# Kernel optimization log

Hardware: AMD Instinct MI355X
Metric: run time of the kernel (lower is better)

The kernel has to match this reference:

```python
import jax, jax.numpy as jnp
import numpy as np

N_MIN = 5
N_MAX = 16
VARIANTS_PER_N = 16
NUM_HIDDEN = 2
HIDDEN = 512
TOTAL_MODELS = (N_MAX - N_MIN + 1) * VARIANTS_PER_N  # 192
BATCH = 65536


def setup_inputs() -> dict:
    key = jax.random.key(0)
    ks = jax.random.split(key, 8)
    n = 16
    s_in = 1.0 / np.sqrt(n)
    s_h = 1.0 / np.sqrt(HIDDEN)
    return {
        "T": jax.random.normal(ks[0], (BATCH, n), dtype=jnp.float32),
        "n": n,
        "variant_index": 3,
        "w_in": jax.random.normal(ks[1], (TOTAL_MODELS, HIDDEN, N_MAX), dtype=jnp.float32) * s_in,
        "b_in": jax.random.normal(ks[2], (TOTAL_MODELS, HIDDEN), dtype=jnp.float32) * 0.01,
        "w_hid": jax.random.normal(ks[3], (TOTAL_MODELS, NUM_HIDDEN, HIDDEN, HIDDEN), dtype=jnp.float32) * s_h,
        "b_hid": jax.random.normal(ks[4], (TOTAL_MODELS, NUM_HIDDEN, HIDDEN), dtype=jnp.float32) * 0.01,
        "w_out": jax.random.normal(ks[5], (TOTAL_MODELS, N_MAX + 1, HIDDEN), dtype=jnp.float32) * s_h,
        "b_out": jax.random.normal(ks[6], (TOTAL_MODELS, N_MAX + 1), dtype=jnp.float32) * 0.01,
    }


def _distortion(X, n):
    # X: (B, n+1). Z[:, n-1-i] = sum_j X[:, j] * X[:, j+i+1] (zero-padded shift).
    # lag k = i+1 -> column n-k; loop is over fixed small n (<=16), unrolls statically.
    cols = [jnp.sum(X[:, :-k] * X[:, k:], axis=1) for k in range(1, n + 1)]
    return jnp.stack(cols[::-1], axis=1)  # (B, n)


def reference(T, n, variant_index, w_in, b_in, w_hid, b_hid, w_out, b_out):
    model_idx = (n - N_MIN) * VARIANTS_PER_N + variant_index
    wi = w_in[model_idx]    # (H, N_MAX)
    bi = b_in[model_idx]    # (H,)
    wh = w_hid[model_idx]   # (2, H, H)
    bh = b_hid[model_idx]   # (2, H)
    wo = w_out[model_idx]   # (N_MAX+1, H)
    bo = b_out[model_idx]   # (N_MAX+1,)

    T_pad = jnp.pad(T, ((0, 0), (0, N_MAX - n)))  # (B, N_MAX)
    norm = jnp.sqrt(jnp.clip(jnp.sum(T_pad * T_pad, axis=1, keepdims=True), 1e-12))
    T_unit = T_pad / norm
    scale = jnp.sqrt(norm)

    x = jax.nn.silu(T_unit @ wi.T + bi)
    for h in range(NUM_HIDDEN):
        x = jax.nn.relu(x @ wh[h].T + bh[h])
    x_full = (x @ wo.T + bo) * scale  # (B, N_MAX+1)

    X_hat = x_full[:, :n + 1]
    X_hat_clamped = jnp.clip(X_hat, -2.0, 2.0)
    error = jnp.mean((_distortion(X_hat, n) - T) ** 2)
    error_clamped = jnp.mean((_distortion(X_hat_clamped, n) - T) ** 2)
    return (X_hat, error, X_hat_clamped, error_clamped)
```

## Files before the change

### kernel.cpp

```cpp
#include <hip/hip_runtime.h>

#define BATCH 65536
#define MT 128
#define NBLK (BATCH / MT)

typedef unsigned short u16;
typedef __bf16 bf16x8 __attribute__((ext_vector_type(8)));
typedef float f32x4 __attribute__((ext_vector_type(4)));

#define WI_OFF 0
#define WH_OFF 16384
#define WO_OFF 540672
#define WS_USH 557056
#define BI_F 0
#define BH_F 512
#define BO_F 1536
#define PART_F 1568
#define PREP_WH 65536
#define PREP_WI 2048
#define PREP_WO 2048
#define PREP_SC 1568
#define PREP_TOTAL (PREP_WH + PREP_WI + PREP_WO + PREP_SC)

__device__ inline u16 f2bf(float f) {
  union { float f; unsigned u; } v; v.f = f;
  unsigned u = v.u + 0x7fffu + ((v.u >> 16) & 1u);
  return (u16)(u >> 16);
}

__global__ void prep_kernel(const float* __restrict__ w_in, const float* __restrict__ b_in,
                            const float* __restrict__ w_hid, const float* __restrict__ b_hid,
                            const float* __restrict__ w_out, const float* __restrict__ b_out,
                            const int* __restrict__ variant, int n,
                            u16* __restrict__ wsu, float* __restrict__ wsf)
{
  const int model = (n - 5) * 16 + variant[0];
  const int i = blockIdx.x * 256 + threadIdx.x;
  if (i < PREP_WH) {
    int g = i & 3, col = (i >> 2) & 511, K32 = (i >> 11) & 15, l = i >> 15;
    const float* src = w_hid + (size_t)model * 524288 + (size_t)l * 262144 + col * 512 + K32 * 32 + g * 8;
    u16* dst = wsu + WH_OFF + (size_t)i * 8;
    #pragma unroll
    for (int e = 0; e < 8; ++e) dst[e] = f2bf(src[e]);
  } else if (i < PREP_WH + PREP_WI) {
    int j = i - PREP_WH;
    int g = j & 3, col = j >> 2;
    u16* dst = wsu + WI_OFF + (size_t)j * 8;
    #pragma unroll
    for (int e = 0; e < 8; ++e) {
      int k = g * 8 + e;
      dst[e] = (k < 16) ? f2bf(w_in[(size_t)model * 8192 + col * 16 + k]) : (u16)0;
    }
  } else if (i < PREP_WH + PREP_WI + PREP_WO) {
    int j = i - PREP_WH - PREP_WI;
    int g = j & 3, col = (j >> 2) & 31, K32 = j >> 7;
    u16* dst = wsu + WO_OFF + (size_t)j * 8;
    #pragma unroll
    for (int e = 0; e < 8; ++e) {
      int k = K32 * 32 + g * 8 + e;
      dst[e] = (col < 17) ? f2bf(w_out[(size_t)model * 8704 + col * 512 + k]) : (u16)0;
    }
  } else if (i < PREP_TOTAL) {
    int j = i - PREP_WH - PREP_WI - PREP_WO;
    if (j < 512)       wsf[BI_F + j] = b_in[(size_t)model * 512 + j];
    else if (j < 1536) wsf[BH_F + (j - 512)] = b_hid[(size_t)model * 1024 + (j - 512)];
    else               { int o = j - 1536; wsf[BO_F + o] = (o < 17) ? b_out[(size_t)model * 17 + o] : 0.f; }
  }
}

__device__ __forceinline__ bf16x8 rdA(const char* xb, int row, int kbyte) {
  return *reinterpret_cast<const bf16x8*>(xb + row * 1024 + (kbyte ^ ((row & 15) << 4)));
}
__device__ __forceinline__ void st16(char* xb, int row, int col, u16 v) {
  *(u16*)(xb + row * 1024 + ((col * 2) ^ ((row & 15) << 4))) = v;
}

template<int NK>
__device__ __forceinline__ void dense_layer(const u16* __restrict__ Wp,
                                            const float* __restrict__ bias, int act,
                                            char* xb, int l15, int q, int r0, int c0)
{
  f32x4 acc[4][8];
  #pragma unroll
  for (int a = 0; a < 4; ++a)
    #pragma unroll
    for (int b = 0; b < 8; ++b) { f32x4 z = {0.f, 0.f, 0.f, 0.f}; acc[a][b] = z; }

  const u16* Wl = Wp + (c0 + l15) * 32 + q * 8;

  if constexpr (NK == 1) {
    uint4 b0[8];
    #pragma unroll
    for (int ct = 0; ct < 8; ++ct)
      b0[ct] = *reinterpret_cast<const uint4*>(Wl + ct * 512);
    const int kb = q * 16;
    #pragma unroll
    for (int mt = 0; mt < 4; ++mt) {
      bf16x8 a = rdA(xb, r0 + mt * 16 + l15, kb);
      #pragma unroll
      for (int ct = 0; ct < 8; ++ct)
        acc[mt][ct] = __builtin_amdgcn_mfma_f32_16x16x32_bf16(
            a, __builtin_bit_cast(bf16x8, b0[ct]), acc[mt][ct], 0, 0, 0);
    }
  } else {
    uint4 bc[8], bn[8];
    #pragma unroll
    for (int ct = 0; ct < 8; ++ct)
      bc[ct] = *reinterpret_cast<const uint4*>(Wl + ct * 512);
    #pragma unroll 1
    for (int i = 0; i < NK; i += 2) {
      {
        const u16* p = Wl + (size_t)(i + 1) * 16384;
        #pragma unroll
        for (int ct = 0; ct < 8; ++ct)
          bn[ct] = *reinterpret_cast<const uint4*>(p + ct * 512);
      }
      {
        const int kb = i * 64 + q * 16;
        #pragma unroll
        for (int mt = 0; mt < 4; ++mt) {
          bf16x8 a = rdA(xb, r0 + mt * 16 + l15, kb);
          #pragma unroll
          for (int ct = 0; ct < 8; ++ct)
            acc[mt][ct] = __builtin_amdgcn_mfma_f32_16x16x32_bf16(
                a, __builtin_bit_cast(bf16x8, bc[ct]), acc[mt][ct], 0, 0, 0);
        }
      }
      {
        const u16* p = Wl + (size_t)((i + 2) & (NK - 1)) * 16384;
        #pragma unroll
        for (int ct = 0; ct < 8; ++ct)
          bc[ct] = *reinterpret_cast<const uint4*>(p + ct * 512);
      }
      {
        const int kb = (i + 1) * 64 + q * 16;
        #pragma unroll
        for (int mt = 0; mt < 4; ++mt) {
          bf16x8 a = rdA(xb, r0 + mt * 16 + l15, kb);
          #pragma unroll
          for (int ct = 0; ct < 8; ++ct)
            acc[mt][ct] = __builtin_amdgcn_mfma_f32_16x16x32_bf16(
                a, __builtin_bit_cast(bf16x8, bn[ct]), acc[mt][ct], 0, 0, 0);
        }
      }
    }
  }
  __syncthreads();

  float bv[8];
  #pragma unroll
  for (int ct = 0; ct < 8; ++ct) bv[ct] = bias[c0 + ct * 16 + l15];
  #pragma unroll
  for (int mt = 0; mt < 4; ++mt)
    #pragma unroll
    for (int ct = 0; ct < 8; ++ct)
      #pragma unroll
      for (int j = 0; j < 4; ++j) {
        int row = r0 + mt * 16 + q * 4 + j;
        float z = acc[mt][ct][j] + bv[ct];
        float h = act ? fmaxf(z, 0.f) : z / (1.f + __expf(-z));
        st16(xb, row, c0 + ct * 16 + l15, f2bf(h));
      }
  __syncthreads();
}

template<int CN>
__global__ __launch_bounds__(512, 2) void fused_kernel(
    const float* __restrict__ T, const u16* __restrict__ wsu,
    const float* __restrict__ wsf, float* __restrict__ Xout, float* __restrict__ Xcout,
    float* __restrict__ errPart, int n_arg)
{
  const int n = CN ? CN : n_arg;
  __shared__ u16 xs[MT * 512];
  __shared__ float xo[MT * 20];
  __shared__ float ts[MT * 16];
  __shared__ float scaleS[MT];
  __shared__ float ered[8][2];

  const int tid = threadIdx.x;
  const int blk = blockIdx.x;
  const int lane = tid & 63;
  const int wid = tid >> 6;
  const int l15 = lane & 15;
  const int q = lane >> 4;
  const int r0 = (wid >> 2) * 64;
  const int c0 = (wid & 3) * 128;
  char* xb = (char*)xs;

  {
    const int r = tid >> 2, j = tid & 3;
    const size_t gr = (size_t)blk * MT + r;
    const float* tp = T + gr * n;
    float v[4]; float ss = 0.f;
    #pragma unroll
    for (int c = 0; c < 4; ++c) {
      int k = j * 4 + c;
      v[c] = (k < n) ? tp[k] : 0.f;
      ss += v[c] * v[c];
    }
    ss += __shfl_xor(ss, 1); ss += __shfl_xor(ss, 2);
    float norm = sqrtf(ss < 1e-12f ? 1e-12f : ss);
    float rn = 1.f / norm;
    if (j == 0) scaleS[r] = sqrtf(norm);
    #pragma unroll
    for (int c = 0; c < 4; ++c) {
      st16(xb, r, j * 4 + c, f2bf(v[c] * rn));
      st16(xb, r, 16 + j * 4 + c, 0);
      ts[r * 16 + j * 4 + c] = v[c];
    }
  }
  __syncthreads();

  dense_layer<1 >(wsu + WI_OFF,          wsf + BI_F,       0, xb, l15, q, r0, c0);
  dense_layer<16>(wsu + WH_OFF,          wsf + BH_F,       1, xb, l15, q, r0, c0);
  dense_layer<16>(wsu + WH_OFF + 262144, wsf + BH_F + 512, 1, xb, l15, q, r0, c0);

  {
    f32x4 oacc[2];
    { f32x4 z = {0.f, 0.f, 0.f, 0.f}; oacc[0] = z; oacc[1] = z; }
    const int bofs2 = l15 * 32 + q * 8;
    uint4 ob[2], on[2];
    #pragma unroll
    for (int ct = 0; ct < 2; ++ct)
      ob[ct] = *reinterpret_cast<const uint4*>(wsu + WO_OFF + bofs2 + ct * 512);
    #pragma unroll 1
    for (int K2 = 0; K2 < 16; K2 += 2) {
      #pragma unroll
      for (int ct = 0; ct < 2; ++ct)
        on[ct] = *reinterpret_cast<const uint4*>(wsu + WO_OFF + (size_t)(K2 + 1) * 1024 + bofs2 + ct * 512);
      {
        bf16x8 a = rdA(xb, wid * 16 + l15, K2 * 64 + q * 16);
        #pragma unroll
        for (int ct = 0; ct < 2; ++ct)
          oacc[ct] = __builtin_amdgcn_mfma_f32_16x16x32_bf16(
              a, __builtin_bit_cast(bf16x8, ob[ct]), oacc[ct], 0, 0, 0);
      }
      #pragma unroll
      for (int ct = 0; ct < 2; ++ct)
        ob[ct] = *reinterpret_cast<const uint4*>(wsu + WO_OFF + (size_t)((K2 + 2) & 15) * 1024 + bofs2 + ct * 512);
      {
        bf16x8 a = rdA(xb, wid * 16 + l15, (K2 + 1) * 64 + q * 16);
        #pragma unroll
        for (int ct = 0; ct < 2; ++ct)
          oacc[ct] = __builtin_amdgcn_mfma_f32_16x16x32_bf16(
              a, __builtin_bit_cast(bf16x8, on[ct]), oacc[ct], 0, 0, 0);
      }
    }
    #pragma unroll
    for (int ct = 0; ct < 2; ++ct)
      #pragma unroll
      for (int j = 0; j < 4; ++j) {
        int o = ct * 16 + l15;
        int row = wid * 16 + q * 4 + j;
        if (o <= n) {
          float val = (oacc[ct][j] + wsf[BO_F + o]) * scaleS[row];
          size_t gr = (size_t)blk * MT + row;
          float cv = fminf(fmaxf(val, -2.f), 2.f);
          Xout[gr * (n + 1) + o] = val;
          Xcout[gr * (n + 1) + o] = cv;
          xo[row * 20 + o] = val;
        }
      }
  }
  __syncthreads();

  {
    const int r = tid >> 2, j = tid & 3;
    float x[17], cx[17];
    #pragma unroll
    for (int i = 0; i < 17; ++i) {
      float v = (i <= n) ? xo[r * 20 + i] : 0.f;
      x[i] = v; cx[i] = fminf(fmaxf(v, -2.f), 2.f);
    }
    float e = 0.f, ec = 0.f;
    #pragma unroll
    for (int kk = 0; kk < 4; ++kk) {
      int k = j + 1 + kk * 4;
      if (k <= n) {
        float d = 0.f, dc = 0.f;
        #pragma unroll
        for (int i = 0; i < 16; ++i) {
          if (i + k <= 16) {
            if (i + k <= n) { d += x[i] * x[i + k]; dc += cx[i] * cx[i + k]; }
          }
        }
        float tvv = ts[r * 16 + (n - k)];
        float r1 = d - tvv, r2 = dc - tvv;
        e += r1 * r1; ec += r2 * r2;
      }
    }
    e += __shfl_xor(e, 1);  ec += __shfl_xor(ec, 1);
    e += __shfl_xor(e, 2);  ec += __shfl_xor(ec, 2);
    e += __shfl_xor(e, 4);  ec += __shfl_xor(ec, 4);
    e += __shfl_xor(e, 8);  ec += __shfl_xor(ec, 8);
    e += __shfl_xor(e, 16); ec += __shfl_xor(ec, 16);
    e += __shfl_xor(e, 32); ec += __shfl_xor(ec, 32);
    if (lane == 0) { ered[wid][0] = e; ered[wid][1] = ec; }
  }
  __syncthreads();
  if (tid == 0) {
    float e = 0.f, ec = 0.f;
    #pragma unroll
    for (int w = 0; w < 8; ++w) { e += ered[w][0]; ec += ered[w][1]; }
    errPart[blk * 2]     = e;
    errPart[blk * 2 + 1] = ec;
  }
}

__global__ void finalize_kernel(const float* __restrict__ part, float* __restrict__ e0,
                                float* __restrict__ e1, float inv)
{
  __shared__ float se[4][2];
  const int t = threadIdx.x;
  float e = 0.f, ec = 0.f;
  for (int b = t; b < NBLK; b += 256) { e += part[2 * b]; ec += part[2 * b + 1]; }
  e += __shfl_xor(e, 1);  ec += __shfl_xor(ec, 1);
  e += __shfl_xor(e, 2);  ec += __shfl_xor(ec, 2);
  e += __shfl_xor(e, 4);  ec += __shfl_xor(ec, 4);
  e += __shfl_xor(e, 8);  ec += __shfl_xor(ec, 8);
  e += __shfl_xor(e, 16); ec += __shfl_xor(ec, 16);
  e += __shfl_xor(e, 32); ec += __shfl_xor(ec, 32);
  if ((t & 63) == 0) { se[t >> 6][0] = e; se[t >> 6][1] = ec; }
  __syncthreads();
  if (t == 0) {
    float te = 0.f, tec = 0.f;
    #pragma unroll
    for (int w = 0; w < 4; ++w) { te += se[w][0]; tec += se[w][1]; }
    e0[0] = te * inv;
    e1[0] = tec * inv;
  }
}

extern "C" void kernel_launch(void* const* d_in, const int* in_sizes, int n_in,
                              void* d_out, int out_size, void* d_ws, size_t ws_size,
                              hipStream_t stream)
{
  const float* T       = (const float*)d_in[0];
  const int*   variant = (const int*)d_in[2];
  const float* w_in    = (const float*)d_in[3];
  const float* b_in    = (const float*)d_in[4];
  const float* w_hid   = (const float*)d_in[5];
  const float* b_hid   = (const float*)d_in[6];
  const float* w_out   = (const float*)d_in[7];
  const float* b_out   = (const float*)d_in[8];
  const int n = in_sizes[0] / BATCH;

  u16* wsu = (u16*)d_ws;
  float* wsf = (float*)((char*)d_ws + (size_t)WS_USH * 2);
  float* out = (float*)d_out;
  const size_t xe = (size_t)BATCH * (n + 1);
  float* Xo  = out;
  float* eP  = out + xe;
  float* Xc  = out + xe + 1;
  float* ecP = out + 2 * xe + 1;

  const int prepBlocks = (PREP_TOTAL + 255) / 256;
  prep_kernel<<<prepBlocks, 256, 0, stream>>>(w_in, b_in, w_hid, b_hid, w_out, b_out,
                                              variant, n, wsu, wsf);
  if (n == 16)
    fused_kernel<16><<<NBLK, 512, 0, stream>>>(T, wsu, wsf, Xo, Xc, wsf + PART_F, n);
  else
    fused_kernel<0><<<NBLK, 512, 0, stream>>>(T, wsu, wsf, Xo, Xc, wsf + PART_F, n);
  finalize_kernel<<<1, 256, 0, stream>>>(wsf + PART_F, eP, ecP, 1.f / (float)((size_t)BATCH * n));
}
```

Before: 152.3 us.

## Split fused MLP into per-layer kernels with global activation buffers

Replaces the single fused kernel, which ran all layers per 128-row tile, with separate layer0, hidden and output kernels working on 64-row tiles. Each hidden layer writes its activations to workspace in global memory, and the next kernel stages them back into LDS with global_load_lds. The aim is smaller LDS use and blocks for higher occupancy, and the removal of intra-block syncs between layers. The cost is roughly 64MB of activation traffic written and read per layer plus extra kernel launches, and each weight tile is now reused across only 64 rows.

```diff
diff --git a/kernel.cpp b/kernel.cpp
--- a/kernel.cpp
+++ b/kernel.cpp
@@ -1,7 +1,7 @@
 #include <hip/hip_runtime.h>
 
 #define BATCH 65536
-#define MT 128
+#define MT 64
 #define NBLK (BATCH / MT)
 
 typedef unsigned short u16;
@@ -15,7 +15,12 @@
 #define BI_F 0
 #define BH_F 512
 #define BO_F 1536
-#define PART_F 1568
+#define PART_F 4096
+#define SCALE_F 8192
+#define X1_OFF (2u * 1024u * 1024u)
+#define X2_OFF (X1_OFF + 67108864u)
+#define X3_OFF (X2_OFF + 67108864u)
+
 #define PREP_WH 65536
 #define PREP_WI 2048
 #define PREP_WO 2048
@@ -71,81 +76,159 @@
 __device__ __forceinline__ bf16x8 rdA(const char* xb, int row, int kbyte) {
   return *reinterpret_cast<const bf16x8*>(xb + row * 1024 + (kbyte ^ ((row & 15) << 4)));
 }
-__device__ __forceinline__ void st16(char* xb, int row, int col, u16 v) {
-  *(u16*)(xb + row * 1024 + ((col * 2) ^ ((row & 15) << 4))) = v;
-}
-
-template<int NK>
-__device__ __forceinline__ void dense_layer(const u16* __restrict__ Wp,
-                                            const float* __restrict__ bias, int act,
-                                            char* xb, int l15, int q, int r0, int c0)
-{
+__device__ __forceinline__ void stG(char* X, size_t grow, int col, u16 v) {
+  *(u16*)(X + grow * 1024 + ((col * 2) ^ (((int)(grow & 15)) << 4))) = v;
+}
+
+__device__ __forceinline__ void stage16(const char* g, const char* l) {
+  __builtin_amdgcn_global_load_lds(
+      (const __attribute__((address_space(1))) unsigned int*)(uintptr_t)g,
+      (__attribute__((address_space(3))) unsigned int*)(unsigned)(uintptr_t)l,
+      16, 0, 0);
+}
+
+template<int CN>
+__global__ __launch_bounds__(256, 2) void layer0_kernel(
+    const float* __restrict__ T, const u16* __restrict__ wsu, const float* __restrict__ wsf,
+    char* __restrict__ X1, float* __restrict__ scaleArr, int n_arg)
+{
+  const int n = CN ? CN : n_arg;
+  __shared__ u16 xs0[64 * 40];
+  const int tid = threadIdx.x, blk = blockIdx.x;
+  const int lane = tid & 63, wid = tid >> 6;
+  const int l15 = lane & 15, q = lane >> 4;
+  const int c0 = wid * 128;
+
+  {
+    const int r = tid >> 2, j = tid & 3;
+    const size_t gr = (size_t)blk * MT + r;
+    float v[4];
+    if (CN == 16) {
+      float4 t4 = reinterpret_cast<const float4*>(T + gr * 16)[j];
+      v[0] = t4.x; v[1] = t4.y; v[2] = t4.z; v[3] = t4.w;
+    } else {
+      #pragma unroll
+      for (int c = 0; c < 4; ++c) { int k = j * 4 + c; v[c] = (k < n) ? T[gr * n + k] : 0.f; }
+    }
+    float ss = v[0]*v[0] + v[1]*v[1] + v[2]*v[2] + v[3]*v[3];
+    ss += __shfl_xor(ss, 1); ss += __shfl_xor(ss, 2);
+    float norm = sqrtf(ss < 1e-12f ? 1e-12f : ss);
+    float rn = 1.f / norm;
+    if (j == 0) scaleArr[gr] = sqrtf(norm);
+    #pragma unroll
+    for (int c = 0; c < 4; ++c) {
+      xs0[r * 40 + j * 4 + c] = f2bf(v[c] * rn);
+      xs0[r * 40 + 16 + j * 4 + c] = 0;
+    }
+  }
+  __syncthreads();
+
   f32x4 acc[4][8];
   #pragma unroll
   for (int a = 0; a < 4; ++a)
     #pragma unroll
-    for (int b = 0; b < 8; ++b) { f32x4 z = {0.f, 0.f, 0.f, 0.f}; acc[a][b] = z; }
-
-  const u16* Wl = Wp + (c0 + l15) * 32 + q * 8;
-
-  if constexpr (NK == 1) {
-    uint4 b0[8];
+    for (int b = 0; b < 8; ++b) { f32x4 z = {0.f,0.f,0.f,0.f}; acc[a][b] = z; }
+
+  const u16* Wl = wsu + WI_OFF + (c0 + l15) * 32 + q * 8;
+  uint4 b0[8];
+  #pragma unroll
+  for (int ct = 0; ct < 8; ++ct)
+    b0[ct] = *reinterpret_cast<const uint4*>(Wl + ct * 512);
+  #pragma unroll
+  for (int mt = 0; mt < 4; ++mt) {
+    bf16x8 a = *reinterpret_cast<const bf16x8*>(&xs0[(mt * 16 + l15) * 40 + q * 8]);
     #pragma unroll
     for (int ct = 0; ct < 8; ++ct)
-      b0[ct] = *reinterpret_cast<const uint4*>(Wl + ct * 512);
-    const int kb = q * 16;
-    #pragma unroll
-    for (int mt = 0; mt < 4; ++mt) {
-      bf16x8 a = rdA(xb, r0 + mt * 16 + l15, kb);
+      acc[mt][ct] = __builtin_amdgcn_mfma_f32_16x16x32_bf16(
+          a, __builtin_bit_cast(bf16x8, b0[ct]), acc[mt][ct], 0, 0, 0);
+  }
+
+  float bv[8];
+  #pragma unroll
+  for (int ct = 0; ct < 8; ++ct) bv[ct] = wsf[BI_F + c0 + ct * 16 + l15];
+  #pragma unroll
+  for (int mt = 0; mt < 4; ++mt)
+    #pragma unroll
+    for (int ct = 0; ct < 8; ++ct)
+      #pragma unroll
+      for (int j = 0; j < 4; ++j) {
+        int rl = mt * 16 + q * 4 + j;
+        size_t gr = (size_t)blk * MT + rl;
+        float z = acc[mt][ct][j] + bv[ct];
+        float h = z / (1.f + __expf(-z));
+        stG(X1, gr, c0 + ct * 16 + l15, f2bf(h));
+      }
+}
+
+__global__ __launch_bounds__(256, 2) void hidden_kernel(
+    const char* __restrict__ Xin, const u16* __restrict__ Wbase,
+    const float* __restrict__ bias, char* __restrict__ Xout)
+{
+  __shared__ u16 xs[MT * 512];
+  const int tid = threadIdx.x, blk = blockIdx.x;
+  const int lane = tid & 63, wid = tid >> 6;
+  const int l15 = lane & 15, q = lane >> 4;
+  const int c0 = wid * 128;
+  char* xb = (char*)xs;
+
+  {
+    const char* src = Xin + (size_t)blk * 65536;
+    #pragma unroll
+    for (int r2 = 0; r2 < 16; ++r2)
+      stage16(src + tid * 16 + r2 * 4096, xb + tid * 16 + r2 * 4096);
+  }
+  asm volatile("s_waitcnt vmcnt(0)" ::: "memory");
+  __syncthreads();
+
+  f32x4 acc[4][8];
+  #pragma unroll
+  for (int a = 0; a < 4; ++a)
+    #pragma unroll
+    for (int b = 0; b < 8; ++b) { f32x4 z = {0.f,0.f,0.f,0.f}; acc[a][b] = z; }
+
+  const u16* Wl = Wbase + (c0 + l15) * 32 + q * 8;
+  uint4 bc[8], bn[8];
+  #pragma unroll
+  for (int ct = 0; ct < 8; ++ct)
+    bc[ct] = *reinterpret_cast<const uint4*>(Wl + ct * 512);
+
+  #pragma unroll 1
+  for (int i = 0; i < 16; i += 2) {
+    {
+      const u16* p = Wl + (size_t)(i + 1) * 16384;
       #pragma unroll
       for (int ct = 0; ct < 8; ++ct)
-        acc[mt][ct] = __builtin_amdgcn_mfma_f32_16x16x32_bf16(
-            a, __builtin_bit_cast(bf16x8, b0[ct]), acc[mt][ct], 0, 0, 0);
-    }
-  } else {
-    uint4 bc[8], bn[8];
-    #pragma unroll
-    for (int ct = 0; ct < 8; ++ct)
-      bc[ct] = *reinterpret_cast<const uint4*>(Wl + ct * 512);
-    #pragma unroll 1
-    for (int i = 0; i < NK; i += 2) {
-      {
-        const u16* p = Wl + (size_t)(i + 1) * 16384;
+        bn[ct] = *reinterpret_cast<const uint4*>(p + ct * 512);
+    }
+    {
+      const int kb = i * 64 + q * 16;
+      #pragma unroll
+      for (int mt = 0; mt < 4; ++mt) {
+        bf16x8 a = rdA(xb, mt * 16 + l15, kb);
         #pragma unroll
         for (int ct = 0; ct < 8; ++ct)
-          bn[ct] = *reinterpret_cast<const uint4*>(p + ct * 512);
-      }
-      {
-        const int kb = i * 64 + q * 16;
-        #pragma unroll
-        for (int mt = 0; mt < 4; ++mt) {
-          bf16x8 a = rdA(xb, r0 + mt * 16 + l15, kb);
-          #pragma unroll
-          for (int ct = 0; ct < 8; ++ct)
-            acc[mt][ct] = __builtin_amdgcn_mfma_f32_16x16x32_bf16(
-                a, __builtin_bit_cast(bf16x8, bc[ct]), acc[mt][ct], 0, 0, 0);
-        }
-      }
-      {
-        const u16* p = Wl + (size_t)((i + 2) & (NK - 1)) * 16384;
+          acc[mt][ct] = __builtin_amdgcn_mfma_f32_16x16x32_bf16(
+              a, __builtin_bit_cast(bf16x8, bc[ct]), acc[mt][ct], 0, 0, 0);
+      }
+    }
+    {
+      const u16* p = Wl + (size_t)((i + 2) & 15) * 16384;
+      #pragma unroll
+      for (int ct = 0; ct < 8; ++ct)
+        bc[ct] = *reinterpret_cast<const uint4*>(p + ct * 512);
+    }
+    {
+      const int kb = (i + 1) * 64 + q * 16;
+      #pragma unroll
+      for (int mt = 0; mt < 4; ++mt) {
+        bf16x8 a = rdA(xb, mt * 16 + l15, kb);
         #pragma unroll
         for (int ct = 0; ct < 8; ++ct)
-          bc[ct] = *reinterpret_cast<const uint4*>(p + ct * 512);
-      }
-      {
-        const int kb = (i + 1) * 64 + q * 16;
-        #pragma unroll
-        for (int mt = 0; mt < 4; ++mt) {
-          bf16x8 a = rdA(xb, r0 + mt * 16 + l15, kb);
-          #pragma unroll
-          for (int ct = 0; ct < 8; ++ct)
-            acc[mt][ct] = __builtin_amdgcn_mfma_f32_16x16x32_bf16(
-                a, __builtin_bit_cast(bf16x8, bn[ct]), acc[mt][ct], 0, 0, 0);
-        }
-      }
-    }
-  }
-  __syncthreads();
+          acc[mt][ct] = __builtin_amdgcn_mfma_f32_16x16x32_bf16(
+              a, __builtin_bit_cast(bf16x8, bn[ct]), acc[mt][ct], 0, 0, 0);
+      }
+    }
+  }
 
   float bv[8];
   #pragma unroll
@@ -156,80 +239,53 @@
     for (int ct = 0; ct < 8; ++ct)
       #pragma unroll
       for (int j = 0; j < 4; ++j) {
-        int row = r0 + mt * 16 + q * 4 + j;
+        int rl = mt * 16 + q * 4 + j;
+        size_t gr = (size_t)blk * MT + rl;
         float z = acc[mt][ct][j] + bv[ct];
-        float h = act ? fmaxf(z, 0.f) : z / (1.f + __expf(-z));
-        st16(xb, row, c0 + ct * 16 + l15, f2bf(h));
-      }
-  __syncthreads();
+        stG(Xout, gr, c0 + ct * 16 + l15, f2bf(fmaxf(z, 0.f)));
+      }
 }
 
 template<int CN>
-__global__ __launch_bounds__(512, 2) void fused_kernel(
-    const float* __restrict__ T, const u16* __restrict__ wsu,
-    const float* __restrict__ wsf, float* __restrict__ Xout, float* __restrict__ Xcout,
+__global__ __launch_bounds__(256, 2) void out_kernel(
+    const float* __restrict__ T, const char* __restrict__ X3,
+    const u16* __restrict__ wsu, const float* __restrict__ wsf,
+    const float* __restrict__ scaleArr, float* __restrict__ Xout, float* __restrict__ Xcout,
     float* __restrict__ errPart, int n_arg)
 {
   const int n = CN ? CN : n_arg;
   __shared__ u16 xs[MT * 512];
   __shared__ float xo[MT * 20];
-  __shared__ float ts[MT * 16];
-  __shared__ float scaleS[MT];
-  __shared__ float ered[8][2];
-
-  const int tid = threadIdx.x;
-  const int blk = blockIdx.x;
-  const int lane = tid & 63;
-  const int wid = tid >> 6;
-  const int l15 = lane & 15;
-  const int q = lane >> 4;
-  const int r0 = (wid >> 2) * 64;
-  const int c0 = (wid & 3) * 128;
+  __shared__ float ered[4][2];
+  const int tid = threadIdx.x, blk = blockIdx.x;
+  const int lane = tid & 63, wid = tid >> 6;
+  const int l15 = lane & 15, q = lane >> 4;
   char* xb = (char*)xs;
 
   {
-    const int r = tid >> 2, j = tid & 3;
-    const size_t gr = (size_t)blk * MT + r;
-    const float* tp = T + gr * n;
-    float v[4]; float ss = 0.f;
-    #pragma unroll
-    for (int c = 0; c < 4; ++c) {
-      int k = j * 4 + c;
-      v[c] = (k < n) ? tp[k] : 0.f;
-      ss += v[c] * v[c];
-    }
-    ss += __shfl_xor(ss, 1); ss += __shfl_xor(ss, 2);
-    float norm = sqrtf(ss < 1e-12f ? 1e-12f : ss);
-    float rn = 1.f / norm;
-    if (j == 0) scaleS[r] = sqrtf(norm);
-    #pragma unroll
-    for (int c = 0; c < 4; ++c) {
-      st16(xb, r, j * 4 + c, f2bf(v[c] * rn));
-      st16(xb, r, 16 + j * 4 + c, 0);
-      ts[r * 16 + j * 4 + c] = v[c];
-    }
-  }
-  __syncthreads();
-
-  dense_layer<1 >(wsu + WI_OFF,          wsf + BI_F,       0, xb, l15, q, r0, c0);
-  dense_layer<16>(wsu + WH_OFF,          wsf + BH_F,       1, xb, l15, q, r0, c0);
-  dense_layer<16>(wsu + WH_OFF + 262144, wsf + BH_F + 512, 1, xb, l15, q, r0, c0);
+    const char* src = X3 + (size_t)blk * 65536;
+    #pragma unroll
+    for (int r2 = 0; r2 < 16; ++r2)
+      stage16(src + tid * 16 + r2 * 4096, xb + tid * 16 + r2 * 4096);
+  }
+  asm volatile("s_waitcnt vmcnt(0)" ::: "memory");
+  __syncthreads();
 
   {
     f32x4 oacc[2];
-    { f32x4 z = {0.f, 0.f, 0.f, 0.f}; oacc[0] = z; oacc[1] = z; }
+    { f32x4 z = {0.f,0.f,0.f,0.f}; oacc[0] = z; oacc[1] = z; }
     const int bofs2 = l15 * 32 + q * 8;
     uint4 ob[2], on[2];
     #pragma unroll
     for (int ct = 0; ct < 2; ++ct)
       ob[ct] = *reinterpret_cast<const uint4*>(wsu + WO_OFF + bofs2 + ct * 512);
     #pragma unroll 1
-    for (int K2 = 0; K2 < 16; K2 += 2) {
+    for (int K = 0; K < 16; K += 2) {
       #pragma unroll
       for (int ct = 0; ct < 2; ++ct)
-        on[ct] = *reinterpret_cast<const uint4*>(wsu + WO_OFF + (size_t)(K2 + 1) * 1024 + bofs2 + ct * 512);
+        on[ct] = *reinterpret_cast<const uint4*>(wsu + WO_OFF + (size_t)(K + 1) * 1024 + bofs2 + ct * 512);
       {
-        bf16x8 a = rdA(xb, wid * 16 + l15, K2 * 64 + q * 16);
+        bf16x8 a = rdA(xb, wid * 16 + l15, K * 64 + q * 16);
         #pragma unroll
         for (int ct = 0; ct < 2; ++ct)
           oacc[ct] = __builtin_amdgcn_mfma_f32_16x16x32_bf16(
@@ -237,9 +293,9 @@
       }
       #pragma unroll
       for (int ct = 0; ct < 2; ++ct)
-        ob[ct] = *reinterpret_cast<const uint4*>(wsu + WO_OFF + (size_t)((K2 + 2) & 15) * 1024 + bofs2 + ct * 512);
+        ob[ct] = *reinterpret_cast<const uint4*>(wsu + WO_OFF + (size_t)((K + 2) & 15) * 1024 + bofs2 + ct * 512);
       {
-        bf16x8 a = rdA(xb, wid * 16 + l15, (K2 + 1) * 64 + q * 16);
+        bf16x8 a = rdA(xb, wid * 16 + l15, (K + 1) * 64 + q * 16);
         #pragma unroll
         for (int ct = 0; ct < 2; ++ct)
           oacc[ct] = __builtin_amdgcn_mfma_f32_16x16x32_bf16(
@@ -251,14 +307,14 @@
       #pragma unroll
       for (int j = 0; j < 4; ++j) {
         int o = ct * 16 + l15;
-        int row = wid * 16 + q * 4 + j;
+        int rl = wid * 16 + q * 4 + j;
+        size_t gr = (size_t)blk * MT + rl;
         if (o <= n) {
-          float val = (oacc[ct][j] + wsf[BO_F + o]) * scaleS[row];
-          size_t gr = (size_t)blk * MT + row;
+          float val = (oacc[ct][j] + wsf[BO_F + o]) * scaleArr[gr];
           float cv = fminf(fmaxf(val, -2.f), 2.f);
           Xout[gr * (n + 1) + o] = val;
           Xcout[gr * (n + 1) + o] = cv;
-          xo[row * 20 + o] = val;
+          xo[rl * 20 + o] = val;
         }
       }
   }
@@ -266,6 +322,7 @@
 
   {
     const int r = tid >> 2, j = tid & 3;
+    const size_t gr = (size_t)blk * MT + r;
     float x[17], cx[17];
     #pragma unroll
     for (int i = 0; i < 17; ++i) {
@@ -284,7 +341,7 @@
             if (i + k <= n) { d += x[i] * x[i + k]; dc += cx[i] * cx[i + k]; }
           }
         }
-        float tvv = ts[r * 16 + (n - k)];
+        float tvv = T[gr * n + (n - k)];
         float r1 = d - tvv, r2 = dc - tvv;
         e += r1 * r1; ec += r2 * r2;
       }
@@ -301,7 +358,7 @@
   if (tid == 0) {
     float e = 0.f, ec = 0.f;
     #pragma unroll
-    for (int w = 0; w < 8; ++w) { e += ered[w][0]; ec += ered[w][1]; }
+    for (int w = 0; w < 4; ++w) { e += ered[w][0]; ec += ered[w][1]; }
     errPart[blk * 2]     = e;
     errPart[blk * 2 + 1] = ec;
   }
@@ -345,8 +402,13 @@
   const float* b_out   = (const float*)d_in[8];
   const int n = in_sizes[0] / BATCH;
 
-  u16* wsu = (u16*)d_ws;
+  u16* wsu  = (u16*)d_ws;
   float* wsf = (float*)((char*)d_ws + (size_t)WS_USH * 2);
+  char* X1 = (char*)d_ws + X1_OFF;
+  char* X2 = (char*)d_ws + X2_OFF;
+  char* X3 = (char*)d_ws + X3_OFF;
+  float* scaleArr = wsf + SCALE_F;
+
   float* out = (float*)d_out;
   const size_t xe = (size_t)BATCH * (n + 1);
   float* Xo  = out;
@@ -358,8 +420,14 @@
   prep_kernel<<<prepBlocks, 256, 0, stream>>>(w_in, b_in, w_hid, b_hid, w_out, b_out,
                                               variant, n, wsu, wsf);
   if (n == 16)
-    fused_kernel<16><<<NBLK, 512, 0, stream>>>(T, wsu, wsf, Xo, Xc, wsf + PART_F, n);
+    layer0_kernel<16><<<NBLK, 256, 0, stream>>>(T, wsu, wsf, X1, scaleArr, n);
   else
-    fused_kernel<0><<<NBLK, 512, 0, stream>>>(T, wsu, wsf, Xo, Xc, wsf + PART_F, n);
+    layer0_kernel<0><<<NBLK, 256, 0, stream>>>(T, wsu, wsf, X1, scaleArr, n);
+  hidden_kernel<<<NBLK, 256, 0, stream>>>(X1, wsu + WH_OFF,          wsf + BH_F,       X2);
+  hidden_kernel<<<NBLK, 256, 0, stream>>>(X2, wsu + WH_OFF + 262144, wsf + BH_F + 512, X3);
+  if (n == 16)
+    out_kernel<16><<<NBLK, 256, 0, stream>>>(T, X3, wsu, wsf, scaleArr, Xo, Xc, wsf + PART_F, n);
+  else
+    out_kernel<0><<<NBLK, 256, 0, stream>>>(T, X3, wsu, wsf, scaleArr, Xo, Xc, wsf + PART_F, n);
   finalize_kernel<<<1, 256, 0, stream>>>(wsf + PART_F, eP, ecP, 1.f / (float)((size_t)BATCH * n));
 }
```

After: 166.8 us. +9.5%, slower.
